# Kernel optimization log

Hardware: AMD Instinct MI355X
Metric: run time of the kernel (lower is better)

Reference implementation:

```python
import jax, jax.numpy as jnp
import numpy as np

BETA1, BETA2, BETA3 = 0.9, 0.8, 0.9
DECAY1, INC1 = 0.05, 5.0
DECAY3, INC3 = 0.05, 5.0
LATENCY = 4.0
B_CONST = 0.15
LIF1_MIN, LIF1_MAX = 150.0, 400.0
LIF3_MIN, LIF3_MAX = 50.0, 200.0
A_P, A_M, TAU_P, TAU_M = 0.01, 0.01, 20.0, 20.0  # exponential STDP params (params1/2/3)


def stdp(dt):
    # exponential STDP curve: potentiate when post fires after pre (dt>=0), depress otherwise
    return jnp.where(dt >= 0, A_P * jnp.exp(-dt / TAU_P), -A_M * jnp.exp(dt / TAU_M))


def setup_inputs() -> dict:
    key = jax.random.key(0)
    k1, k2, k3, k4 = jax.random.split(key, 4)
    H, N, C = 8192, 4096, 128
    return {
        "image": jax.random.uniform(k1, (N,), jnp.float32),
        "W1": jax.random.uniform(k2, (H, N), jnp.float32),
        "W2": jax.random.uniform(k3, (N, H), jnp.float32),
        "W3": jax.random.uniform(k4, (C, N), jnp.float32),
        "thr1": 100.0 * jnp.ones((H,), jnp.float32),
        "thr2": 5.0 * jnp.ones((N,), jnp.float32),
        "thr3": 100.0 * jnp.ones((C,), jnp.float32),
        "time": 256,
        "pw": 8,
    }


def reference(image, W1, W2, W3, thr1, thr2, thr3, time, pw):
    N = image.shape[0]
    H = W1.shape[0]
    C = W3.shape[0]
    T = int(time)
    Tf = jnp.float32(T)

    img_t = Tf * image  # input spike times, [N]
    # rate -> pulse encoding: input_spikes[t, i] = 1 for t in [floor(img_t[i]), floor(img_t[i])+pw)
    t_axis = jnp.arange(T, dtype=jnp.float32)[:, None]          # [T,1]
    start = jnp.floor(img_t)[None, :]                            # [1,N]
    input_spikes = ((t_axis >= start) & (t_axis < start + pw)).astype(jnp.float32)  # [T,N]

    def wta(mem, th):
        # winner-take-all (snntorch inhibition=True): only argmax neuron may spike
        j = jnp.argmax(mem)
        fire = (mem[j] > th[j]).astype(mem.dtype)
        return fire * jax.nn.one_hot(j, mem.shape[0], dtype=mem.dtype)

    def step(carry, xs):
        mem1, mem2, mem3, th1, th3, r1, r2, r3, hid_act, out_act = carry
        x, t = xs
        # layer 1: Leaky LIF, inhibition, reset-to-zero
        mem1 = BETA1 * mem1 + jnp.dot(W1, x)
        spk1 = wta(mem1, th1)
        mem1 = mem1 * (1.0 - spk1)
        # layer 2: Leaky LIF, no inhibition, reset-by-subtract
        mem2 = BETA2 * mem2 + jnp.dot(W2, spk1)
        spk2 = (mem2 > thr2).astype(mem2.dtype)
        mem2 = mem2 - spk2 * thr2
        # layer 3 (clustering): Leaky LIF, inhibition, zeroed after any spike
        mem3 = BETA3 * mem3 + jnp.dot(W3, spk2)
        spk3 = wta(mem3, th3)
        mem3 = mem3 - spk3 * th3
        mem3 = jnp.where(jnp.sum(spk3) > 0, 0.0, mem3)
        # first-spike-time recon (recon stays at first nonzero spk*(t+1))
        r1 = jnp.where(r1 != 0, r1, spk1 * (t + 1.0))
        r2 = jnp.where(r2 != 0, r2, spk2 * (t + 1.0))
        r3 = jnp.where(r3 != 0, r3, spk3 * (t + 1.0))
        hid_act = hid_act + spk1
        out_act = out_act + spk2
        # adaptive thresholds: homeostatic decay + spike-triggered increase, clamped
        th1 = jnp.clip(th1 - DECAY1 + INC1 * spk1, LIF1_MIN, LIF1_MAX)
        th3 = jnp.clip(th3 - DECAY3 + INC3 * spk3, LIF3_MIN, LIF3_MAX)
        return (mem1, mem2, mem3, th1, th3, r1, r2, r3, hid_act, out_act), None

    z = jnp.zeros
    carry0 = (z(H), z(N), z(C), thr1, thr3, z(H), z(N), z(C), z(H), z(N))
    (mem1, mem2, mem3, th1, th3, r1, r2, r3, hid_act, out_act), _ = jax.lax.scan(
        step, carry0, (input_spikes, jnp.arange(T, dtype=jnp.float32)))

    # neurons that never spiked get time T
    r1 = jnp.where(r1 == 0, Tf, r1)
    r2 = jnp.where(r2 == 0, Tf, r2)
    r3 = jnp.where(r3 == 0, Tf, r3)

    # STDP weight updates (exponential), same structure as PresentImage
    hid_mask = (hid_act > 0).astype(jnp.float32)
    delta_t1 = (r1[:, None] - img_t[None, :]) * hid_mask[:, None]      # [H,N]
    W1_new = W1 + stdp(delta_t1)
    delta_t2 = r2[:, None] - r1[None, :]                                # [N,H]
    zeta = (Tf - r1) * hid_mask / Tf                                    # [H]
    rho = (r2 - LATENCY - img_t) / Tf + B_CONST                         # [N]
    W2_new = jnp.clip(W2 + stdp(delta_t2) * (rho[:, None] * zeta[None, :]), 0.0, 1.0)
    delta_t3 = r3[:, None] - r2[None, :]                                # [C,N]
    W3_new = W3 + stdp(delta_t3)

    error = (img_t - (r2 - LATENCY)) / Tf
    error_scalar = jnp.sum(jnp.square(error))
    return (error, error_scalar, r1, r2, r3, W1_new, W2_new, W3_new)
```

## Files before the change

kernel.cpp:

```cpp
#include <hip/hip_runtime.h>
#include <cstdint>
#include <cstddef>

#define Hn 8192
#define Nn 4096
#define Cn 128
#define Tt 256
#define CAP 192

typedef unsigned long long ull;

__device__ __forceinline__ float th_lazy2(float b, float lo, float hi, int nup){
    if (nup <= 0) return b;
    float a = fminf(fmaxf(__fsub_rn(b, 0.05f), lo), hi);
    if (nup == 1) return a;
    return fmaxf(__fsub_rn(a, __fmul_rn(0.05f, (float)(nup - 1))), lo);
}

__device__ __forceinline__ float clamp01(float v){
    return fminf(fmaxf(v, 0.f), 1.f);
}

template<int CTRL>
__device__ __forceinline__ int dpp_i(int x, int old){
    return __builtin_amdgcn_update_dpp(old, x, CTRL, 0xf, 0xf, false);
}
__device__ __forceinline__ float wave_max_f(float v){
    const int NEG = __float_as_int(-3.4e38f);
#define STEPM(C) { float o = __int_as_float(dpp_i<C>(__float_as_int(v), NEG)); v = fmaxf(v, o); }
    STEPM(0x111) STEPM(0x112) STEPM(0x114) STEPM(0x118) STEPM(0x142) STEPM(0x143)
#undef STEPM
    return __int_as_float(__builtin_amdgcn_readlane(__float_as_int(v), 63));
}
__device__ __forceinline__ int wave_argmax_l(float bv, int bh, float &wv, int &wh){
    float v = wave_max_f(bv);
    ull tie = __ballot(bv == v);
    int tl = __ffsll((long long)tie) - 1;
    int h = __builtin_amdgcn_readlane(bh, tl);
    if (__builtin_expect(__popcll(tie) > 1, 0)){
        ull m = tie & (tie - 1);
        while (m){
            int l2 = __ffsll((long long)m) - 1;
            int h2 = __builtin_amdgcn_readlane(bh, l2);
            if (h2 < h){ h = h2; tl = l2; }
            m &= m - 1;
        }
    }
    wv = v; wh = h; return tl;
}
__device__ __forceinline__ float rl_f(float x, int l){
    return __int_as_float(__builtin_amdgcn_readlane(__float_as_int(x), l));
}

__global__ __launch_bounds__(1024) void k_prep(const float* __restrict__ image,
        int* __restrict__ boff, int* __restrict__ sidx, unsigned* __restrict__ anyv,
        float* __restrict__ imgt, float* __restrict__ eiP, float* __restrict__ eiM){
    __shared__ int s_start[Nn];
    __shared__ int s_c4[4][Tt];
    __shared__ int s_boff[Tt + 1];
    int tid = threadIdx.x;
    for (int i = tid; i < Nn; i += 1024){
        float im = image[i];
        float img = __fmul_rn(256.f, im);
        s_start[i] = (int)floorf(img);
        imgt[i] = img;
        eiP[i] = __expf(img * 0.05f);
        eiM[i] = __expf(-img * 0.05f);
    }
    if (tid < Tt) anyv[tid] = 0u;
    __syncthreads();
    int b = tid & 255, q = tid >> 8;
    {
        int c = 0;
        for (int k = 0; k < 1024; ++k) c += (s_start[q * 1024 + k] == b) ? 1 : 0;
        s_c4[q][b] = c;
    }
    __syncthreads();
    if (tid == 0){
        int acc = 0;
        for (int bb = 0; bb < Tt; ++bb){
            s_boff[bb] = acc;
            acc += s_c4[0][bb] + s_c4[1][bb] + s_c4[2][bb] + s_c4[3][bb];
        }
        s_boff[Tt] = acc;
    }
    __syncthreads();
    if (tid <= Tt) boff[tid] = s_boff[tid];
    int p = s_boff[b];
    if (q > 0) p += s_c4[0][b];
    if (q > 1) p += s_c4[1][b];
    if (q > 2) p += s_c4[2][b];
    for (int k = 0; k < 1024; ++k){
        int i = q * 1024 + k;
        if (s_start[i] == b) sidx[p++] = i;
    }
}

__global__ __launch_bounds__(256) void k_gbuckets(const float* __restrict__ W1,
        const int* __restrict__ boff, const int* __restrict__ sidx,
        float* __restrict__ G_T){
    __shared__ float rows[2][Nn];
    int tid = threadIdx.x;
    int h0 = blockIdx.x * 2;
    for (int r = 0; r < 2; ++r){
        const float4* src = (const float4*)(W1 + (size_t)(h0 + r) * Nn);
        float4* dst = (float4*)rows[r];
        for (int j = tid; j < Nn / 4; j += 256) dst[j] = src[j];
    }
    __syncthreads();
    int t = tid;
    int b0 = boff[t], b1 = boff[t + 1];
    float s0 = 0.f, s1 = 0.f;
    for (int k = b0; k < b1; ++k){
        int i = sidx[k];
        s0 += rows[0][i]; s1 += rows[1][i];
    }
    G_T[(size_t)(h0 + 0) * Tt + t] = s0;
    G_T[(size_t)(h0 + 1) * Tt + t] = s1;
}

__global__ __launch_bounds__(256) void k_w1bulk(const float* __restrict__ W1,
        float* __restrict__ o_W1){
    size_t base = (size_t)blockIdx.x * 4096;
    const float4* src = (const float4*)W1;
    float4* dst = (float4*)o_W1;
    for (int i = threadIdx.x; i < 4096; i += 256){
        float4 s = src[base + i];
        s.x = __fadd_rn(s.x, 0.01f); s.y = __fadd_rn(s.y, 0.01f);
        s.z = __fadd_rn(s.z, 0.01f); s.w = __fadd_rn(s.w, 0.01f);
        dst[base + i] = s;
    }
}

__global__ __launch_bounds__(256) void k_c1M(const float* __restrict__ G_T,
        float* __restrict__ M, float* __restrict__ r1pre, float* __restrict__ o_r1){
    __shared__ float tile[32][Tt + 1];
    __shared__ float c1s[32][Tt + 1];
    const int tid = threadIdx.x;
    const int h0 = blockIdx.x * 32;
    for (int r = 0; r < 32; ++r) tile[r][tid] = G_T[(size_t)(h0 + r) * Tt + tid];
    __syncthreads();
    {
        int hs = tid & 31, ts = tid >> 5;
        for (int tb = 0; tb < 32; ++tb){
            int t = tb * 8 + ts;
            int lo = (t - 7 < 0) ? 0 : t - 7;
            float s = 0.f;
            for (int u = lo; u <= t; ++u) s += tile[hs][u];
            c1s[hs][t] = s;
        }
    }
    __syncthreads();
    if (tid < 32){
        float m = 0.f;
        for (int t = 0; t < Tt; ++t){
            m = __fadd_rn(__fmul_rn(0.9f, m), c1s[tid][t]);
            M[(size_t)t * Hn + h0 + tid] = m;
        }
        r1pre[h0 + tid] = 0.f;
        o_r1[h0 + tid] = 256.f;
    }
}

__global__ __launch_bounds__(256) void k_sel(const float* __restrict__ M,
        float4* __restrict__ cand){
    const int t = blockIdx.x, tid = threadIdx.x;
    __shared__ float s_row[Hn];
    __shared__ unsigned s_hist[256];
    __shared__ unsigned s_suf[256];
    __shared__ unsigned s_pref;
    __shared__ int s_rank;
    __shared__ int s_cnt;
    __shared__ int s_idx[CAP + 64];
    {
        const float4* src = (const float4*)(M + (size_t)t * Hn);
        float4* d4 = (float4*)s_row;
        for (int j = tid; j < Hn / 4; j += 256) d4[j] = src[j];
    }
    if (tid == 0){ s_pref = 0u; s_rank = CAP; s_cnt = 0; }
    __syncthreads();
#pragma unroll
    for (int b = 3; b >= 0; --b){
        s_hist[tid] = 0u;
        __syncthreads();
        unsigned pref = s_pref;
        int r = s_rank;
        for (int k = 0; k < 32; ++k){
            unsigned u = __float_as_uint(s_row[tid + (k << 8)]);
            bool match = (b == 3) ? true : ((u >> ((b + 1) * 8)) == pref);
            if (match) atomicAdd(&s_hist[(u >> (b * 8)) & 255], 1u);
        }
        __syncthreads();
        s_suf[tid] = s_hist[tid];
        __syncthreads();
#pragma unroll
        for (int off = 1; off < 256; off <<= 1){
            unsigned v = (tid + off < 256) ? s_suf[tid + off] : 0u;
            __syncthreads();
            s_suf[tid] += v;
            __syncthreads();
        }
        unsigned above = s_suf[tid] - s_hist[tid];
        if ((int)above < r && r <= (int)s_suf[tid]){
            s_pref = (pref << 8) | (unsigned)tid;
            s_rank = r - (int)above;
        }
        __syncthreads();
    }
    unsigned V = s_pref;
    for (int k = 0; k < 32; ++k){
        int i = tid + (k << 8);
        unsigned u = __float_as_uint(s_row[i]);
        if (u >= V){
            int p = atomicAdd(&s_cnt, 1);
            if (p < CAP + 64) s_idx[p] = i;
        }
    }
    __syncthreads();
    int c = s_cnt;
    bool ovf = (c > CAP);
    float vV = ovf ? 3.4e38f : __uint_as_float(V);
    for (int i = tid; i < CAP; i += 256){
        float4 e;
        if (!ovf && i < c){
            int ix = s_idx[i];
            e = make_float4(s_row[ix], __int_as_float(ix | (1 << 15)), 0.f, vV);
        } else {
            e = make_float4(-1.f, 0.f, 0.f, vV);
        }
        cand[(size_t)t * CAP + i] = e;
    }
}

#define NB_W2 2048
#define NB_W3T 128

union FusedLDS {
    struct {
        float4 mst[Hn];
        int j1[Tt];
        unsigned bm[256];
    } w;
    float tl[64][65];
};

__global__ __launch_bounds__(512, 1) void k_fused(
        const float* __restrict__ M, const float4* __restrict__ cand,
        const float* __restrict__ thr1,
        const float* __restrict__ W2, const float* __restrict__ W3,
        float* __restrict__ o_W2, float* __restrict__ W3T,
        float* __restrict__ r1pre, float* __restrict__ o_r1,
        int* __restrict__ j1s, int* __restrict__ mh, int* __restrict__ nRout){
    __shared__ FusedLDS u;
    const int bid = blockIdx.x;
    const int tid = threadIdx.x;

    if (bid >= 1 && bid < 1 + NB_W2){
        size_t base = (size_t)(bid - 1) * 4096;
        const float4* src = (const float4*)W2;
        float4* dst = (float4*)o_W2;
        for (int i = tid; i < 4096; i += 2048){
            float4 a0 = src[base + i];
            float4 a1 = src[base + i + 512];
            float4 a2 = src[base + i + 1024];
            float4 a3 = src[base + i + 1536];
            a0.x = clamp01(a0.x); a0.y = clamp01(a0.y); a0.z = clamp01(a0.z); a0.w = clamp01(a0.w);
            a1.x = clamp01(a1.x); a1.y = clamp01(a1.y); a1.z = clamp01(a1.z); a1.w = clamp01(a1.w);
            a2.x = clamp01(a2.x); a2.y = clamp01(a2.y); a2.z = clamp01(a2.z); a2.w = clamp01(a2.w);
            a3.x = clamp01(a3.x); a3.y = clamp01(a3.y); a3.z = clamp01(a3.z); a3.w = clamp01(a3.w);
            dst[base + i]        = a0;
            dst[base + i + 512]  = a1;
            dst[base + i + 1024] = a2;
            dst[base + i + 1536] = a3;
        }
        return;
    }
    if (bid >= 1 + NB_W2){
        int r = bid - 1 - NB_W2;
        int bx = r & 63, by = r >> 6;
        int n0 = bx * 64, c0 = by * 64;
        for (int e = tid; e < 64 * 64; e += 512){
            int rr = e >> 6, cc = e & 63;
            u.tl[rr][cc] = W3[(size_t)(c0 + rr) * Nn + n0 + cc];
        }
        __syncthreads();
        for (int e = tid; e < 64 * 64; e += 512){
            int rn = e >> 6, cc = e & 63;
            W3T[(size_t)(n0 + rn) * Cn + c0 + cc] = u.tl[cc][rn];
        }
        return;
    }

    for (int h = tid; h < Hn; h += 512)
        u.w.mst[h] = make_float4(0.f, -1.f, thr1[h], 0.f);
    __syncthreads();
    if (tid >= 64) return;
    const int lane = tid;
    const float Lc = -0.15200309344504997f;

    float4 cA0 = cand[lane],         cA1 = cand[64 + lane],         cA2 = cand[128 + lane];
    float4 cB0 = cand[CAP + lane],   cB1 = cand[CAP + 64 + lane],   cB2 = cand[CAP + 128 + lane];
    float4 cC0 = cand[2*CAP + lane], cC1 = cand[2*CAP + 64 + lane], cC2 = cand[2*CAP + 128 + lane];
    float4 gA0, gA1, gA2;
    {
        int h0 = __float_as_int(cA0.y) & 8191;
        int h1 = __float_as_int(cA1.y) & 8191;
        int h2 = __float_as_int(cA2.y) & 8191;
        gA0 = u.w.mst[h0]; gA1 = u.w.mst[h1]; gA2 = u.w.mst[h2];
    }

    for (int t = 0; t < Tt; ++t){
        const float tf = (float)t;
        float bm = -3.4e38f; int bhh = 0x7FFFFFFF;
        float braw = 0.f, bts = 0.f, bthb = 0.f;
#define CPROC(c) { \
        int mc = __float_as_int(cA##c.y); \
        int hc = mc & 8191; \
        float dd = __fsub_rn(tf, gA##c.y); \
        float mem = __fsub_rn(cA##c.x, __fmul_rn(exp2f(__fmul_rn(dd, Lc)), gA##c.x)); \
        if (!((mc >> 15) & 1)) mem = -3.4e38f; \
        if (mem > bm || (mem == bm && hc < bhh)){ bm = mem; bhh = hc; braw = cA##c.x; bts = gA##c.y; bthb = gA##c.z; } }
        CPROC(0) CPROC(1) CPROC(2)
#undef CPROC
        const int hB0 = __float_as_int(cB0.y) & 8191;
        const int hB1 = __float_as_int(cB1.y) & 8191;
        const int hB2 = __float_as_int(cB2.y) & 8191;
        float4 gB0 = u.w.mst[hB0];
        float4 gB1 = u.w.mst[hB1];
        float4 gB2 = u.w.mst[hB2];
        float wv; int wh;
        int wl = wave_argmax_l(bm, bhh, wv, wh);
        float raw = rl_f(braw, wl), tsv = rl_f(bts, wl), thb = rl_f(bthb, wl);
        const float vc = cA0.w;
        int skip = 0;
        if (__builtin_expect(wv < vc, 0)){
            if (t > 0 && vc < 150.f){
                skip = 1;
            } else {
                float fv = -3.4e38f; int fh = 0x7FFFFFFF;
                float fraw = 0.f, fts = 0.f, fthb = 0.f;
                const float4* Mrow4 = (const float4*)(M + (size_t)t * Hn);
                for (int q = 0; q < 32; ++q){
                    int e = q * 64 + lane;
                    float4 mv = Mrow4[e];
                    int ib = e * 4;
                    float4 g0 = u.w.mst[ib+0], g1 = u.w.mst[ib+1], g2 = u.w.mst[ib+2], g3 = u.w.mst[ib+3];
#define FPROC(comp, gg, o2) { float x = mv.comp; float dd = __fsub_rn(tf, gg.y); \
                    float mm = __fsub_rn(x, __fmul_rn(exp2f(__fmul_rn(dd, Lc)), gg.x)); \
                    int h2 = ib + o2; \
                    if (mm > fv || (mm == fv && h2 < fh)){ fv = mm; fh = h2; fraw = x; fts = gg.y; fthb = gg.z; } }
                    FPROC(x, g0, 0) FPROC(y, g1, 1) FPROC(z, g2, 2) FPROC(w, g3, 3)
#undef FPROC
                }
                wl = wave_argmax_l(fv, fh, wv, wh);
                raw = rl_f(fraw, wl); tsv = rl_f(fts, wl); thb = rl_f(fthb, wl);
            }
        }
        int fire = 0; float thnew = 0.f;
        if (!skip){
            float te = th_lazy2(thb, 150.f, 400.f, t - (int)tsv - 1);
            if (wv > te){
                fire = 1;
                thnew = fminf(fmaxf(__fadd_rn(__fsub_rn(te, 0.05f), 5.0f), 150.f), 400.f);
            }
        }
        if (fire){
            if (lane == 0){
                u.w.j1[t] = wh;
                if (tsv < 0.f){ o_r1[wh] = tf + 1.f; r1pre[wh] = tf + 1.f; }
                u.w.mst[wh] = make_float4(raw, tf, thnew, 0.f);
            }
            float4 upd = make_float4(raw, tf, thnew, 0.f);
            if (hB0 == wh) gB0 = upd;
            if (hB1 == wh) gB1 = upd;
            if (hB2 == wh) gB2 = upd;
        } else {
            if (lane == 0) u.w.j1[t] = -1;
        }
        cA0 = cB0; cA1 = cB1; cA2 = cB2;
        cB0 = cC0; cB1 = cC1; cB2 = cC2;
        int tn = (t + 3 < Tt) ? t + 3 : Tt - 1;
        cC0 = cand[(size_t)tn * CAP + lane];
        cC1 = cand[(size_t)tn * CAP + 64 + lane];
        cC2 = cand[(size_t)tn * CAP + 128 + lane];
        gA0 = gB0; gA1 = gB1; gA2 = gB2;
    }

    for (int i = lane; i < 256; i += 64) u.w.bm[i] = 0u;
    asm volatile("s_waitcnt lgkmcnt(0)" ::: "memory");
    for (int i = lane; i < Tt; i += 64){
        int h = u.w.j1[i];
        j1s[i] = h;
        if (h >= 0) atomicOr(&u.w.bm[h >> 5], 1u << (h & 31));
    }
    asm volatile("s_waitcnt lgkmcnt(0)" ::: "memory");
    unsigned w0 = u.w.bm[lane*4+0], w1 = u.w.bm[lane*4+1];
    unsigned w2 = u.w.bm[lane*4+2], w3 = u.w.bm[lane*4+3];
    int c = __popc(w0) + __popc(w1) + __popc(w2) + __popc(w3);
    int inc = c;
#pragma unroll
    for (int off = 1; off < 64; off <<= 1){
        int v = __shfl_up(inc, off);
        if (lane >= off) inc += v;
    }
    int b = inc - c;
#define WALK(wrd, k) { unsigned ww = wrd; while (ww){ int bt = __ffs(ww) - 1; ww &= ww - 1; \
        mh[b++] = ((lane * 4 + k) << 5) | bt; } }
    WALK(w0, 0) WALK(w1, 1) WALK(w2, 2) WALK(w3, 3)
#undef WALK
    if (lane == 63) *nRout = inc;
}

__global__ __launch_bounds__(64) void k_lif2(const float* __restrict__ W2,
        const int* __restrict__ j1s, const float* __restrict__ thr2,
        float* __restrict__ o_r2, ull* __restrict__ spkb, unsigned* __restrict__ anyv){
    __shared__ int s_j[Tt];
    int lane = threadIdx.x, blk = blockIdx.x;
    for (int i = lane; i < Tt; i += 64) s_j[i] = j1s[i];
    __syncthreads();
    int n = blk * 64 + lane;
    const float* Wrow = W2 + (size_t)n * Hn;
    float tv = thr2[n], m = 0.f, rp = 0.f;
#define LD(dst, tt) { int hh = s_j[tt]; dst = (hh >= 0) ? Wrow[hh] : 0.f; }
#define STEP(uu, tt) { m = __fadd_rn(__fmul_rn(0.8f, m), uu); int f = 0; \
        if (m > tv){ m = __fsub_rn(m, tv); if (rp == 0.f) rp = (float)((tt) + 1); f = 1; } \
        ull mask = __ballot(f); \
        if (lane == 0){ spkb[(tt) * 64 + blk] = mask; if (mask) atomicOr(&anyv[tt], 1u); } }
    float u0, u1, u2, u3;
    LD(u0, 0) LD(u1, 1) LD(u2, 2) LD(u3, 3)
    for (int g = 0; g < 64; ++g){
        float v0 = 0.f, v1 = 0.f, v2 = 0.f, v3 = 0.f;
        if (g < 63){
            int bb = (g + 1) * 4;
            LD(v0, bb) LD(v1, bb + 1) LD(v2, bb + 2) LD(v3, bb + 3)
        }
        int t = g * 4;
        STEP(u0, t) STEP(u1, t + 1) STEP(u2, t + 2) STEP(u3, t + 3)
        u0 = v0; u1 = v1; u2 = v2; u3 = v3;
    }
#undef LD
#undef STEP
    o_r2[n] = (rp == 0.f) ? 256.f : rp;
}

__global__ __launch_bounds__(128, 1) void k_sim3(const ull* __restrict__ spkb,
        const unsigned* __restrict__ anyv, const float* __restrict__ W3T,
        const float* __restrict__ thr3, float* __restrict__ o_r3){
    int tid = threadIdx.x, lane = tid & 63, w = tid >> 6;
    __shared__ ull s_spk[Tt * 64];
    __shared__ unsigned s_any[Tt];
    __shared__ ull s_r2[2];
    __shared__ int s_fire;
    {
        const uint4* src = (const uint4*)spkb;
        uint4* dst = (uint4*)s_spk;
        for (int i = tid; i < Tt * 64 / 2; i += 128) dst[i] = src[i];
    }
    for (int i = tid; i < Tt; i += 128) s_any[i] = anyv[i];
    float m = 0.f, th0 = thr3[tid], rp = 0.f, thv = 0.f;
    int ts = -1, zero = 1;
    __syncthreads();
    for (int t = 0; t < Tt; ++t){
        if (zero && s_any[t] == 0u) continue;
        float d = 0.f;
        if (s_any[t]){
            for (int ww = 0; ww < 64; ++ww){
                ull bits = s_spk[t * 64 + ww];
                while (bits){
                    int b2 = __ffsll((long long)bits) - 1;
                    bits &= bits - 1;
                    d = __fadd_rn(d, W3T[(size_t)(ww * 64 + b2) * Cn + tid]);
                }
            }
        }
        m = __fadd_rn(__fmul_rn(0.9f, m), d);
        ull k = (((ull)__float_as_uint(m >= 0.f ? m : 0.f)) << 32) | (unsigned)(8191 - tid);
        if (!(m >= 0.f)) k = (unsigned)(8191 - tid);
#pragma unroll
        for (int off = 32; off >= 1; off >>= 1){
            ull o = __shfl_down(k, off);
            if (o > k) k = o;
        }
        if (lane == 0) s_r2[w] = k;
        __syncthreads();
        ull wk = s_r2[0] > s_r2[1] ? s_r2[0] : s_r2[1];
        int wc = 8191 - (int)(wk & 0xFFFFu);
        float wv = __uint_as_float((unsigned)(wk >> 32));
        if (tid == wc){
            float te = (ts < 0) ? th_lazy2(th0, 50.f, 200.f, t)
                                : th_lazy2(thv, 50.f, 200.f, t - ts - 1);
            int f = (wv > te) ? 1 : 0;
            s_fire = f;
            if (f){
                thv = fminf(fmaxf(__fadd_rn(__fsub_rn(te, 0.05f), 5.0f), 50.f), 200.f);
                ts = t;
                if (rp == 0.f) rp = (float)(t + 1);
            }
        }
        __syncthreads();
        if (s_fire){ m = 0.f; zero = 1; }
        else zero = 0;
        __syncthreads();
    }
    o_r3[tid] = (rp == 0.f) ? 256.f : rp;
}

__global__ __launch_bounds__(256) void k_post(const float* __restrict__ image,
        const float* __restrict__ r1pre, const float* __restrict__ o_r1,
        const float* __restrict__ o_r2, const float* __restrict__ o_r3,
        const float* __restrict__ imgt, const float* __restrict__ eiP,
        const float* __restrict__ eiM,
        const float* __restrict__ W1, const float* __restrict__ W3,
        const int* __restrict__ mh, const int* __restrict__ nRout,
        float* __restrict__ zeta, float* __restrict__ rho,
        float* __restrict__ Pv, float* __restrict__ Qv,
        float* __restrict__ o_err, float* __restrict__ o_es,
        float* __restrict__ o_W1, float* __restrict__ o_W3){
    const int bid = blockIdx.x;
    const int tid = threadIdx.x;
    if (bid == 0){
        for (int h = tid; h < Hn; h += 256){
            float r1f = o_r1[h];
            float mask = (r1pre[h] != 0.f) ? 1.f : 0.f;
            float z = __fmul_rn(__fmul_rn(__fsub_rn(256.f, r1f), mask), 0.00390625f);
            zeta[h] = z;
            Pv[h] = __expf(r1f * 0.05f) * z;
            Qv[h] = __expf(-r1f * 0.05f) * z;
        }
        float acc = 0.f;
        for (int n = tid; n < Nn; n += 256){
            float img = __fmul_rn(256.f, image[n]);
            float r2f = o_r2[n];
            float e = __fmul_rn(__fsub_rn(img, __fsub_rn(r2f, 4.0f)), 0.00390625f);
            o_err[n] = e;
            rho[n] = __fadd_rn(__fmul_rn(__fsub_rn(__fsub_rn(r2f, 4.0f), img), 0.00390625f), 0.15f);
            acc = __fadd_rn(acc, __fmul_rn(e, e));
        }
        __shared__ float red[4];
        for (int off = 32; off >= 1; off >>= 1) acc += __shfl_down(acc, off);
        int lane = tid & 63, w = tid >> 6;
        if (lane == 0) red[w] = acc;
        __syncthreads();
        if (tid == 0) *o_es = red[0] + red[1] + red[2] + red[3];
        return;
    }
    if (bid <= 256){
        int slot = bid - 1;
        if (slot >= *nRout) return;
        int h = mh[slot];
        float r1f = o_r1[h];
        float a = 0.01f * __expf(-r1f * 0.05f);
        float b = 0.01f * __expf( r1f * 0.05f);
        const float4* src = (const float4*)(W1 + (size_t)h * Nn);
        float4* dst = (float4*)(o_W1 + (size_t)h * Nn);
        const float4* ig = (const float4*)imgt;
        const float4* p4 = (const float4*)eiP;
        const float4* m4 = (const float4*)eiM;
        for (int i = tid; i < Nn / 4; i += 256){
            float4 s = src[i];
            float4 im = ig[i], pp = p4[i], mm = m4[i];
            s.x += (r1f >= im.x) ? a * pp.x : -(b * mm.x);
            s.y += (r1f >= im.y) ? a * pp.y : -(b * mm.y);
            s.z += (r1f >= im.z) ? a * pp.z : -(b * mm.z);
            s.w += (r1f >= im.w) ? a * pp.w : -(b * mm.w);
            dst[i] = s;
        }
        return;
    }
    {
        int cc = bid - 257;
        float r3f = o_r3[cc];
        float a = 0.01f * __expf(-r3f * 0.05f);
        float b = 0.01f * __expf( r3f * 0.05f);
        const float4* src = (const float4*)(W3 + (size_t)cc * Nn);
        float4* dst = (float4*)(o_W3 + (size_t)cc * Nn);
        const float4* r24 = (const float4*)o_r2;
        for (int i = tid; i < Nn / 4; i += 256){
            float4 s = src[i]; float4 rv = r24[i];
            s.x += (r3f >= rv.x) ? a * __expf(rv.x * 0.05f) : -(b * __expf(-rv.x * 0.05f));
            s.y += (r3f >= rv.y) ? a * __expf(rv.y * 0.05f) : -(b * __expf(-rv.y * 0.05f));
            s.z += (r3f >= rv.z) ? a * __expf(rv.z * 0.05f) : -(b * __expf(-rv.z * 0.05f));
            s.w += (r3f >= rv.w) ? a * __expf(rv.w * 0.05f) : -(b * __expf(-rv.w * 0.05f));
            dst[i] = s;
        }
    }
}

__global__ __launch_bounds__(128) void k_w2fix(
        const float* __restrict__ o_r1, const float* __restrict__ Pv,
        const float* __restrict__ Qv, const float* __restrict__ o_r2,
        const float* __restrict__ rho, const int* __restrict__ mh,
        const int* __restrict__ nRout, float* __restrict__ o_W2){
    __shared__ int   s_h[Tt];
    __shared__ float s_rv[Tt], s_pp[Tt], s_qq[Tt];
    int n = blockIdx.x, tid = threadIdx.x;
    int nRv = *nRout;
    for (int s = tid; s < nRv; s += 128){
        int h = mh[s];
        s_h[s] = h; s_rv[s] = o_r1[h]; s_pp[s] = Pv[h]; s_qq[s] = Qv[h];
    }
    __syncthreads();
    float r2f = o_r2[n], rh = rho[n];
    float A = 0.01f * rh * __expf(-r2f * 0.05f);
    float B = 0.01f * rh * __expf( r2f * 0.05f);
    for (int s = tid; s < nRv; s += 128){
        size_t idx = (size_t)n * Hn + s_h[s];
        float w = o_W2[idx];
        float rv = s_rv[s];
        w = clamp01(w + ((r2f >= rv) ? A * s_pp[s] : -(B * s_qq[s])));
        o_W2[idx] = w;
    }
}

extern "C" void kernel_launch(void* const* d_in, const int* in_sizes, int n_in,
                              void* d_out, int out_size, void* d_ws, size_t ws_size,
                              hipStream_t stream){
    const float* image = (const float*)d_in[0];
    const float* W1   = (const float*)d_in[1];
    const float* W2   = (const float*)d_in[2];
    const float* W3   = (const float*)d_in[3];
    const float* thr1 = (const float*)d_in[4];
    const float* thr2 = (const float*)d_in[5];
    const float* thr3 = (const float*)d_in[6];

    float* out  = (float*)d_out;
    float* o_err = out;
    float* o_es  = out + 4096;
    float* o_r1  = out + 4097;
    float* o_r2  = out + 12289;
    float* o_r3  = out + 16385;
    float* o_W1  = out + 16513;
    float* o_W2  = o_W1 + (size_t)Hn * Nn;
    float* o_W3  = o_W2 + (size_t)Nn * Hn;

    float* ws = (float*)d_ws;
    float* G_T   = ws;
    float* M     = G_T + (size_t)Hn * Tt;
    float* W3T   = M + (size_t)Tt * Hn;
    float4* cand = (float4*)(W3T + (size_t)Nn * Cn);
    ull* spkb    = (ull*)(cand + (size_t)Tt * CAP);
    float* r1pre = (float*)(spkb + (size_t)Tt * 64);
    float* zeta  = r1pre + Hn;
    float* rho   = zeta + Hn;
    float* imgt  = rho + Nn;
    float* eiP   = imgt + Nn;
    float* eiM   = eiP + Nn;
    float* Pv    = eiM + Nn;
    float* Qv    = Pv + Hn;
    int* boff   = (int*)(Qv + Hn);
    int* sidx   = boff + (Tt + 1);
    int* j1s    = sidx + Nn;
    int* mh     = j1s + Tt;
    int* nRout  = mh + 256;
    unsigned* anyv = (unsigned*)(nRout + 1);

    k_prep<<<1, 1024, 0, stream>>>(image, boff, sidx, anyv, imgt, eiP, eiM);
    k_gbuckets<<<Hn / 2, 256, 0, stream>>>(W1, boff, sidx, G_T);
    k_w1bulk<<<2048, 256, 0, stream>>>(W1, o_W1);
    k_c1M<<<Hn / 32, 256, 0, stream>>>(G_T, M, r1pre, o_r1);
    k_sel<<<Tt, 256, 0, stream>>>(M, cand);
    k_fused<<<1 + NB_W2 + NB_W3T, 512, 0, stream>>>(
        M, cand, thr1, W2, W3, o_W2, W3T, r1pre, o_r1, j1s, mh, nRout);
    k_lif2<<<Nn / 64, 64, 0, stream>>>(W2, j1s, thr2, o_r2, spkb, anyv);
    k_sim3<<<1, 128, 0, stream>>>(spkb, anyv, W3T, thr3, o_r3);
    k_post<<<1 + 256 + 128, 256, 0, stream>>>(image, r1pre, o_r1, o_r2, o_r3,
        imgt, eiP, eiM, W1, W3, mh, nRout, zeta, rho, Pv, Qv, o_err, o_es, o_W1, o_W3);
    k_w2fix<<<Nn, 128, 0, stream>>>(o_r1, Pv, Qv, o_r2, rho, mh, nRout, o_W2);
}
```

Measured before the change: 560.7 us.

## Stage WTA candidates through LDS ring buffer and fuse W1 copy into gbuckets

The serial layer-1 winner-take-all loop now reads candidates from an LDS ring buffer. Extra waves in the block fill that buffer one chunk ahead, replacing the per-lane register prefetch of global memory. Candidate records shrink from float4 to float2, with the per-step cutoff value moved to a separate array, which halves that traffic. The W1 plus-STDP output copy is folded into k_gbuckets, which reuses the rows already in LDS instead of rereading W1 in a separate kernel. The fused kernel moves to 1024 threads with half as many W2 blocks. In exchange, each chunk adds a block-wide barrier, and the next-step register prefetch with in-place update of the winner's state is dropped.

```diff
diff --git a/kernel.cpp b/kernel.cpp
--- a/kernel.cpp
+++ b/kernel.cpp
@@ -7,6 +7,8 @@
 #define Cn 128
 #define Tt 256
 #define CAP 192
+#define CHUNK 8
+#define RING 16
 
 typedef unsigned long long ull;
 
@@ -98,7 +100,7 @@
 
 __global__ __launch_bounds__(256) void k_gbuckets(const float* __restrict__ W1,
         const int* __restrict__ boff, const int* __restrict__ sidx,
-        float* __restrict__ G_T){
+        float* __restrict__ G_T, float* __restrict__ o_W1){
     __shared__ float rows[2][Nn];
     int tid = threadIdx.x;
     int h0 = blockIdx.x * 2;
@@ -117,18 +119,15 @@
     }
     G_T[(size_t)(h0 + 0) * Tt + t] = s0;
     G_T[(size_t)(h0 + 1) * Tt + t] = s1;
-}
-
-__global__ __launch_bounds__(256) void k_w1bulk(const float* __restrict__ W1,
-        float* __restrict__ o_W1){
-    size_t base = (size_t)blockIdx.x * 4096;
-    const float4* src = (const float4*)W1;
-    float4* dst = (float4*)o_W1;
-    for (int i = threadIdx.x; i < 4096; i += 256){
-        float4 s = src[base + i];
-        s.x = __fadd_rn(s.x, 0.01f); s.y = __fadd_rn(s.y, 0.01f);
-        s.z = __fadd_rn(s.z, 0.01f); s.w = __fadd_rn(s.w, 0.01f);
-        dst[base + i] = s;
+    for (int r = 0; r < 2; ++r){
+        const float4* srw = (const float4*)rows[r];
+        float4* dw = (float4*)(o_W1 + (size_t)(h0 + r) * Nn);
+        for (int j = tid; j < Nn / 4; j += 256){
+            float4 s = srw[j];
+            s.x = __fadd_rn(s.x, 0.01f); s.y = __fadd_rn(s.y, 0.01f);
+            s.z = __fadd_rn(s.z, 0.01f); s.w = __fadd_rn(s.w, 0.01f);
+            dw[j] = s;
+        }
     }
 }
 
@@ -163,7 +162,7 @@
 }
 
 __global__ __launch_bounds__(256) void k_sel(const float* __restrict__ M,
-        float4* __restrict__ cand){
+        float2* __restrict__ cand2, float* __restrict__ gvcap){
     const int t = blockIdx.x, tid = threadIdx.x;
     __shared__ float s_row[Hn];
     __shared__ unsigned s_hist[256];
@@ -219,34 +218,36 @@
     __syncthreads();
     int c = s_cnt;
     bool ovf = (c > CAP);
-    float vV = ovf ? 3.4e38f : __uint_as_float(V);
+    if (tid == 0) gvcap[t] = ovf ? 3.4e38f : __uint_as_float(V);
     for (int i = tid; i < CAP; i += 256){
-        float4 e;
+        float2 e;
         if (!ovf && i < c){
             int ix = s_idx[i];
-            e = make_float4(s_row[ix], __int_as_float(ix | (1 << 15)), 0.f, vV);
+            e = make_float2(s_row[ix], __int_as_float(ix | (1 << 15)));
         } else {
-            e = make_float4(-1.f, 0.f, 0.f, vV);
-        }
-        cand[(size_t)t * CAP + i] = e;
-    }
-}
-
-#define NB_W2 2048
+            e = make_float2(-1.f, 0.f);
+        }
+        cand2[(size_t)t * CAP + i] = e;
+    }
+}
+
+#define NB_W2 1024
 #define NB_W3T 128
 
 union FusedLDS {
     struct {
         float4 mst[Hn];
+        float2 ring[RING][CAP];
+        float  vcr[RING];
         int j1[Tt];
         unsigned bm[256];
     } w;
     float tl[64][65];
 };
 
-__global__ __launch_bounds__(512, 1) void k_fused(
-        const float* __restrict__ M, const float4* __restrict__ cand,
-        const float* __restrict__ thr1,
+__global__ __launch_bounds__(1024, 1) void k_fused(
+        const float* __restrict__ M, const float2* __restrict__ cand2,
+        const float* __restrict__ gvcap, const float* __restrict__ thr1,
         const float* __restrict__ W2, const float* __restrict__ W3,
         float* __restrict__ o_W2, float* __restrict__ W3T,
         float* __restrict__ r1pre, float* __restrict__ o_r1,
@@ -256,22 +257,22 @@
     const int tid = threadIdx.x;
 
     if (bid >= 1 && bid < 1 + NB_W2){
-        size_t base = (size_t)(bid - 1) * 4096;
+        size_t base = (size_t)(bid - 1) * 8192;
         const float4* src = (const float4*)W2;
         float4* dst = (float4*)o_W2;
-        for (int i = tid; i < 4096; i += 2048){
+        for (int i = tid; i < 8192; i += 4096){
             float4 a0 = src[base + i];
-            float4 a1 = src[base + i + 512];
-            float4 a2 = src[base + i + 1024];
-            float4 a3 = src[base + i + 1536];
+            float4 a1 = src[base + i + 1024];
+            float4 a2 = src[base + i + 2048];
+            float4 a3 = src[base + i + 3072];
             a0.x = clamp01(a0.x); a0.y = clamp01(a0.y); a0.z = clamp01(a0.z); a0.w = clamp01(a0.w);
             a1.x = clamp01(a1.x); a1.y = clamp01(a1.y); a1.z = clamp01(a1.z); a1.w = clamp01(a1.w);
             a2.x = clamp01(a2.x); a2.y = clamp01(a2.y); a2.z = clamp01(a2.z); a2.w = clamp01(a2.w);
             a3.x = clamp01(a3.x); a3.y = clamp01(a3.y); a3.z = clamp01(a3.z); a3.w = clamp01(a3.w);
             dst[base + i]        = a0;
-            dst[base + i + 512]  = a1;
-            dst[base + i + 1024] = a2;
-            dst[base + i + 1536] = a3;
+            dst[base + i + 1024] = a1;
+            dst[base + i + 2048] = a2;
+            dst[base + i + 3072] = a3;
         }
         return;
     }
@@ -279,112 +280,114 @@
         int r = bid - 1 - NB_W2;
         int bx = r & 63, by = r >> 6;
         int n0 = bx * 64, c0 = by * 64;
-        for (int e = tid; e < 64 * 64; e += 512){
+        for (int e = tid; e < 64 * 64; e += 1024){
             int rr = e >> 6, cc = e & 63;
             u.tl[rr][cc] = W3[(size_t)(c0 + rr) * Nn + n0 + cc];
         }
         __syncthreads();
-        for (int e = tid; e < 64 * 64; e += 512){
+        for (int e = tid; e < 64 * 64; e += 1024){
             int rn = e >> 6, cc = e & 63;
             W3T[(size_t)(n0 + rn) * Cn + c0 + cc] = u.tl[cc][rn];
         }
         return;
     }
 
-    for (int h = tid; h < Hn; h += 512)
+    for (int h = tid; h < Hn; h += 1024)
         u.w.mst[h] = make_float4(0.f, -1.f, thr1[h], 0.f);
-    __syncthreads();
+    for (int e = tid; e < CHUNK * CAP; e += 1024){
+        int so = e / CAP, j = e - so * CAP;
+        u.w.ring[so][j] = cand2[(size_t)so * CAP + j];
+    }
+    if (tid < CHUNK) u.w.vcr[tid] = gvcap[tid];
+    __syncthreads();
+
+    const int lane = tid & 63;
+    const float Lc = -0.15200309344504997f;
+
+    for (int c = 0; c < Tt / CHUNK; ++c){
+        if (tid >= 64 && c + 1 < Tt / CHUNK){
+            for (int e = tid - 64; e < CHUNK * CAP; e += 960){
+                int so = e / CAP, j = e - so * CAP;
+                int step = (c + 1) * CHUNK + so;
+                u.w.ring[step & (RING - 1)][j] = cand2[(size_t)step * CAP + j];
+            }
+            if (tid - 64 < CHUNK){
+                int step = (c + 1) * CHUNK + (tid - 64);
+                u.w.vcr[step & (RING - 1)] = gvcap[step];
+            }
+        }
+        if (tid < 64){
+            for (int s = 0; s < CHUNK; ++s){
+                const int t = c * CHUNK + s;
+                const int slot = t & (RING - 1);
+                const float tf = (float)t;
+                float2 e0 = u.w.ring[slot][lane];
+                float2 e1 = u.w.ring[slot][64 + lane];
+                float2 e2 = u.w.ring[slot][128 + lane];
+                float vc = u.w.vcr[slot];
+                int m0b = __float_as_int(e0.y), m1b = __float_as_int(e1.y), m2b = __float_as_int(e2.y);
+                int h0 = m0b & 8191, h1 = m1b & 8191, h2 = m2b & 8191;
+                float4 g0 = u.w.mst[h0];
+                float4 g1 = u.w.mst[h1];
+                float4 g2 = u.w.mst[h2];
+                float bm = -3.4e38f; int bhh = 0x7FFFFFFF;
+                float braw = 0.f, bts = 0.f, bthb = 0.f;
+#define CPROC(ee, mb, hh, gg) { \
+                float dd = __fsub_rn(tf, gg.y); \
+                float mem = __fsub_rn(ee.x, __fmul_rn(exp2f(__fmul_rn(dd, Lc)), gg.x)); \
+                if (!((mb >> 15) & 1)) mem = -3.4e38f; \
+                if (mem > bm || (mem == bm && hh < bhh)){ bm = mem; bhh = hh; braw = ee.x; bts = gg.y; bthb = gg.z; } }
+                CPROC(e0, m0b, h0, g0) CPROC(e1, m1b, h1, g1) CPROC(e2, m2b, h2, g2)
+#undef CPROC
+                float wv; int wh;
+                int wl = wave_argmax_l(bm, bhh, wv, wh);
+                float raw = rl_f(braw, wl), tsv = rl_f(bts, wl), thb = rl_f(bthb, wl);
+                int skip = 0;
+                if (__builtin_expect(wv < vc, 0)){
+                    if (t > 0 && vc < 150.f){
+                        skip = 1;
+                    } else {
+                        float fv = -3.4e38f; int fh = 0x7FFFFFFF;
+                        float fraw = 0.f, fts = 0.f, fthb = 0.f;
+                        const float4* Mrow4 = (const float4*)(M + (size_t)t * Hn);
+                        for (int q = 0; q < 32; ++q){
+                            int e = q * 64 + lane;
+                            float4 mv = Mrow4[e];
+                            int ib = e * 4;
+                            float4 q0 = u.w.mst[ib+0], q1 = u.w.mst[ib+1], q2 = u.w.mst[ib+2], q3 = u.w.mst[ib+3];
+#define FPROC(comp, gg, o2) { float x = mv.comp; float dd = __fsub_rn(tf, gg.y); \
+                            float mm = __fsub_rn(x, __fmul_rn(exp2f(__fmul_rn(dd, Lc)), gg.x)); \
+                            int hh2 = ib + o2; \
+                            if (mm > fv || (mm == fv && hh2 < fh)){ fv = mm; fh = hh2; fraw = x; fts = gg.y; fthb = gg.z; } }
+                            FPROC(x, q0, 0) FPROC(y, q1, 1) FPROC(z, q2, 2) FPROC(w, q3, 3)
+#undef FPROC
+                        }
+                        wl = wave_argmax_l(fv, fh, wv, wh);
+                        raw = rl_f(fraw, wl); tsv = rl_f(fts, wl); fthb = rl_f(fthb, wl); thb = fthb;
+                    }
+                }
+                int fire = 0; float thnew = 0.f;
+                if (!skip){
+                    float te = th_lazy2(thb, 150.f, 400.f, t - (int)tsv - 1);
+                    if (wv > te){
+                        fire = 1;
+                        thnew = fminf(fmaxf(__fadd_rn(__fsub_rn(te, 0.05f), 5.0f), 150.f), 400.f);
+                    }
+                }
+                if (fire){
+                    if (lane == 0){
+                        u.w.j1[t] = wh;
+                        if (tsv < 0.f){ o_r1[wh] = tf + 1.f; r1pre[wh] = tf + 1.f; }
+                        u.w.mst[wh] = make_float4(raw, tf, thnew, 0.f);
+                    }
+                } else {
+                    if (lane == 0) u.w.j1[t] = -1;
+                }
+            }
+        }
+        __syncthreads();
+    }
     if (tid >= 64) return;
-    const int lane = tid;
-    const float Lc = -0.15200309344504997f;
-
-    float4 cA0 = cand[lane],         cA1 = cand[64 + lane],         cA2 = cand[128 + lane];
-    float4 cB0 = cand[CAP + lane],   cB1 = cand[CAP + 64 + lane],   cB2 = cand[CAP + 128 + lane];
-    float4 cC0 = cand[2*CAP + lane], cC1 = cand[2*CAP + 64 + lane], cC2 = cand[2*CAP + 128 + lane];
-    float4 gA0, gA1, gA2;
-    {
-        int h0 = __float_as_int(cA0.y) & 8191;
-        int h1 = __float_as_int(cA1.y) & 8191;
-        int h2 = __float_as_int(cA2.y) & 8191;
-        gA0 = u.w.mst[h0]; gA1 = u.w.mst[h1]; gA2 = u.w.mst[h2];
-    }
-
-    for (int t = 0; t < Tt; ++t){
-        const float tf = (float)t;
-        float bm = -3.4e38f; int bhh = 0x7FFFFFFF;
-        float braw = 0.f, bts = 0.f, bthb = 0.f;
-#define CPROC(c) { \
-        int mc = __float_as_int(cA##c.y); \
-        int hc = mc & 8191; \
-        float dd = __fsub_rn(tf, gA##c.y); \
-        float mem = __fsub_rn(cA##c.x, __fmul_rn(exp2f(__fmul_rn(dd, Lc)), gA##c.x)); \
-        if (!((mc >> 15) & 1)) mem = -3.4e38f; \
-        if (mem > bm || (mem == bm && hc < bhh)){ bm = mem; bhh = hc; braw = cA##c.x; bts = gA##c.y; bthb = gA##c.z; } }
-        CPROC(0) CPROC(1) CPROC(2)
-#undef CPROC
-        const int hB0 = __float_as_int(cB0.y) & 8191;
-        const int hB1 = __float_as_int(cB1.y) & 8191;
-        const int hB2 = __float_as_int(cB2.y) & 8191;
-        float4 gB0 = u.w.mst[hB0];
-        float4 gB1 = u.w.mst[hB1];
-        float4 gB2 = u.w.mst[hB2];
-        float wv; int wh;
-        int wl = wave_argmax_l(bm, bhh, wv, wh);
-        float raw = rl_f(braw, wl), tsv = rl_f(bts, wl), thb = rl_f(bthb, wl);
-        const float vc = cA0.w;
-        int skip = 0;
-        if (__builtin_expect(wv < vc, 0)){
-            if (t > 0 && vc < 150.f){
-                skip = 1;
-            } else {
-                float fv = -3.4e38f; int fh = 0x7FFFFFFF;
-                float fraw = 0.f, fts = 0.f, fthb = 0.f;
-                const float4* Mrow4 = (const float4*)(M + (size_t)t * Hn);
-                for (int q = 0; q < 32; ++q){
-                    int e = q * 64 + lane;
-                    float4 mv = Mrow4[e];
-                    int ib = e * 4;
-                    float4 g0 = u.w.mst[ib+0], g1 = u.w.mst[ib+1], g2 = u.w.mst[ib+2], g3 = u.w.mst[ib+3];
-#define FPROC(comp, gg, o2) { float x = mv.comp; float dd = __fsub_rn(tf, gg.y); \
-                    float mm = __fsub_rn(x, __fmul_rn(exp2f(__fmul_rn(dd, Lc)), gg.x)); \
-                    int h2 = ib + o2; \
-                    if (mm > fv || (mm == fv && h2 < fh)){ fv = mm; fh = h2; fraw = x; fts = gg.y; fthb = gg.z; } }
-                    FPROC(x, g0, 0) FPROC(y, g1, 1) FPROC(z, g2, 2) FPROC(w, g3, 3)
-#undef FPROC
-                }
-                wl = wave_argmax_l(fv, fh, wv, wh);
-                raw = rl_f(fraw, wl); tsv = rl_f(fts, wl); thb = rl_f(fthb, wl);
-            }
-        }
-        int fire = 0; float thnew = 0.f;
-        if (!skip){
-            float te = th_lazy2(thb, 150.f, 400.f, t - (int)tsv - 1);
-            if (wv > te){
-                fire = 1;
-                thnew = fminf(fmaxf(__fadd_rn(__fsub_rn(te, 0.05f), 5.0f), 150.f), 400.f);
-            }
-        }
-        if (fire){
-            if (lane == 0){
-                u.w.j1[t] = wh;
-                if (tsv < 0.f){ o_r1[wh] = tf + 1.f; r1pre[wh] = tf + 1.f; }
-                u.w.mst[wh] = make_float4(raw, tf, thnew, 0.f);
-            }
-            float4 upd = make_float4(raw, tf, thnew, 0.f);
-            if (hB0 == wh) gB0 = upd;
-            if (hB1 == wh) gB1 = upd;
-            if (hB2 == wh) gB2 = upd;
-        } else {
-            if (lane == 0) u.w.j1[t] = -1;
-        }
-        cA0 = cB0; cA1 = cB1; cA2 = cB2;
-        cB0 = cC0; cB1 = cC1; cB2 = cC2;
-        int tn = (t + 3 < Tt) ? t + 3 : Tt - 1;
-        cC0 = cand[(size_t)tn * CAP + lane];
-        cC1 = cand[(size_t)tn * CAP + 64 + lane];
-        cC2 = cand[(size_t)tn * CAP + 128 + lane];
-        gA0 = gB0; gA1 = gB1; gA2 = gB2;
-    }
 
     for (int i = lane; i < 256; i += 64) u.w.bm[i] = 0u;
     asm volatile("s_waitcnt lgkmcnt(0)" ::: "memory");
@@ -637,8 +640,9 @@
     float* G_T   = ws;
     float* M     = G_T + (size_t)Hn * Tt;
     float* W3T   = M + (size_t)Tt * Hn;
-    float4* cand = (float4*)(W3T + (size_t)Nn * Cn);
-    ull* spkb    = (ull*)(cand + (size_t)Tt * CAP);
+    float2* cand2 = (float2*)(W3T + (size_t)Nn * Cn);
+    float* gvcap = (float*)(cand2 + (size_t)Tt * CAP);
+    ull* spkb    = (ull*)(gvcap + Tt);
     float* r1pre = (float*)(spkb + (size_t)Tt * 64);
     float* zeta  = r1pre + Hn;
     float* rho   = zeta + Hn;
@@ -655,12 +659,11 @@
     unsigned* anyv = (unsigned*)(nRout + 1);
 
     k_prep<<<1, 1024, 0, stream>>>(image, boff, sidx, anyv, imgt, eiP, eiM);
-    k_gbuckets<<<Hn / 2, 256, 0, stream>>>(W1, boff, sidx, G_T);
-    k_w1bulk<<<2048, 256, 0, stream>>>(W1, o_W1);
+    k_gbuckets<<<Hn / 2, 256, 0, stream>>>(W1, boff, sidx, G_T, o_W1);
     k_c1M<<<Hn / 32, 256, 0, stream>>>(G_T, M, r1pre, o_r1);
-    k_sel<<<Tt, 256, 0, stream>>>(M, cand);
-    k_fused<<<1 + NB_W2 + NB_W3T, 512, 0, stream>>>(
-        M, cand, thr1, W2, W3, o_W2, W3T, r1pre, o_r1, j1s, mh, nRout);
+    k_sel<<<Tt, 256, 0, stream>>>(M, cand2, gvcap);
+    k_fused<<<1 + NB_W2 + NB_W3T, 1024, 0, stream>>>(
+        M, cand2, gvcap, thr1, W2, W3, o_W2, W3T, r1pre, o_r1, j1s, mh, nRout);
     k_lif2<<<Nn / 64, 64, 0, stream>>>(W2, j1s, thr2, o_r2, spkb, anyv);
     k_sim3<<<1, 128, 0, stream>>>(spkb, anyv, W3T, thr3, o_r3);
     k_post<<<1 + 256 + 128, 256, 0, stream>>>(image, r1pre, o_r1, o_r2, o_r3,
```

Result: faster. 504.0 us (-10.1%).
